# Performance work log

Hardware: AMD Instinct MI355X
Metric: run time of the kernel (lower is better)

## Reference

```python
import jax, jax.numpy as jnp
import numpy as np

B, H, S, D = 2, 16, 2048, 64


def setup_inputs() -> dict:
    key = jax.random.key(0)
    kq, kk, kv = jax.random.split(key, 3)
    Q = jax.random.normal(kq, (B, H, S, D), dtype=jnp.float32)
    K = jax.random.normal(kk, (B, H, S, D), dtype=jnp.float32)
    V = jax.random.normal(kv, (B, H, S, D), dtype=jnp.float32)
    scale = jnp.float32(1.0 / np.sqrt(D))
    # causal mask (1 = keep, 0 = masked), broadcast over batch/heads
    mask = jnp.tril(jnp.ones((S, S), dtype=jnp.int32))[None, None]
    return {"Q": Q, "K": K, "V": V, "scale": scale, "mask": mask}


def reference(Q, K, V, scale, mask):
    # scores: [B,H,S,S] -- intentionally materialized, matching the module
    scores = jnp.einsum("bhqd,bhkd->bhqk", Q, K) * scale
    scores = jnp.where(mask == 0, jnp.float32(-jnp.inf), scores)
    attention_weights = jax.nn.softmax(scores, axis=-1)
    # dropout is identity in eval mode (reference baseline is deterministic)
    output = jnp.einsum("bhqk,bhkd->bhqd", attention_weights, V)
    return output, attention_weights
```

## Files before the change

### kernel.cpp

```cpp
#include <hip/hip_runtime.h>
#include <hip/hip_bf16.h>

#define S_LEN 2048
#define D_DIM 64
#define BH    32
#define BQ    64
#define BK    64
#define NQT   (S_LEN/BQ)
#define KSTR  72
#define NEL   ((size_t)BH * S_LEN * D_DIM)

typedef __attribute__((ext_vector_type(4))) short  short4v;
typedef __attribute__((ext_vector_type(8))) short  short8;
typedef __attribute__((ext_vector_type(4))) float  floatx4;
typedef __attribute__((ext_vector_type(4))) unsigned int uintx4;

__device__ __forceinline__ unsigned short f2bf(float f) {
    unsigned int u = __builtin_bit_cast(unsigned int, f);
    u += 0x7FFFu + ((u >> 16) & 1u);
    return (unsigned short)(u >> 16);
}
__device__ __forceinline__ float bf2f(short s) {
    return __builtin_bit_cast(float, ((unsigned int)(unsigned short)s) << 16);
}

__device__ __forceinline__ short8 load8(const float* p) {
    floatx4 a = *(const floatx4*)p;
    floatx4 b = *(const floatx4*)(p + 4);
    short8 r;
    r[0]=(short)f2bf(a[0]); r[1]=(short)f2bf(a[1]); r[2]=(short)f2bf(a[2]); r[3]=(short)f2bf(a[3]);
    r[4]=(short)f2bf(b[0]); r[5]=(short)f2bf(b[1]); r[6]=(short)f2bf(b[2]); r[7]=(short)f2bf(b[3]);
    return r;
}
__device__ __forceinline__ short8 load8(const __hip_bfloat16* p) {
    return *(const short8*)p;
}
__device__ __forceinline__ void loadrow8(const float* p, unsigned short o[8]) {
    floatx4 a = *(const floatx4*)p, b = *(const floatx4*)(p + 4);
    o[0]=f2bf(a[0]); o[1]=f2bf(a[1]); o[2]=f2bf(a[2]); o[3]=f2bf(a[3]);
    o[4]=f2bf(b[0]); o[5]=f2bf(b[1]); o[6]=f2bf(b[2]); o[7]=f2bf(b[3]);
}
__device__ __forceinline__ void loadrow8(const __hip_bfloat16* p, unsigned short o[8]) {
    short8 v = *(const short8*)p;
#pragma unroll
    for (int j = 0; j < 8; ++j) o[j] = (unsigned short)v[j];
}

template<typename TIN>
__device__ __forceinline__ void prep_body(const TIN* __restrict__ Q, const TIN* __restrict__ K,
                                          const TIN* __restrict__ V,
                                          unsigned short* __restrict__ Qb,
                                          unsigned short* __restrict__ Kb,
                                          unsigned short* __restrict__ Vtg,
                                          unsigned short (*Lt)[KSTR])
{
    const int tid = threadIdx.x;
    const int bid = blockIdx.x;
    {
        size_t idx = ((size_t)bid * 256 + tid) * 16;
        *(short8*)(Qb + idx)     = load8(Q + idx);
        *(short8*)(Qb + idx + 8) = load8(Q + idx + 8);
        *(short8*)(Kb + idx)     = load8(K + idx);
        *(short8*)(Kb + idx + 8) = load8(K + idx + 8);
    }
    const int bh = bid >> 5, st = bid & 31;
    const TIN* Vb = V + ((size_t)bh * S_LEN + (size_t)st * 64) * D_DIM;
#pragma unroll
    for (int i = 0; i < 2; ++i) {
        int flat = tid * 8 + i * 2048;
        int r = flat >> 6, c = flat & 63;
        short8 v = load8(Vb + (size_t)r * D_DIM + c);
        *(short8*)(&Lt[r][c]) = v;
    }
    __syncthreads();
    unsigned short* Vh = Vtg + (size_t)bh * D_DIM * S_LEN;
#pragma unroll
    for (int i = 0; i < 4; ++i) {
        int flat = tid * 4 + i * 1024;
        int d = flat >> 6, sj = flat & 63;
        short4v o;
        o[0] = (short)Lt[sj+0][d]; o[1] = (short)Lt[sj+1][d];
        o[2] = (short)Lt[sj+2][d]; o[3] = (short)Lt[sj+3][d];
        *(short4v*)(Vh + (size_t)d * S_LEN + (size_t)st * 64 + sj) = o;
    }
}

__global__ __launch_bounds__(256)
void prep_kernel(const void* __restrict__ Q, const void* __restrict__ K,
                 const void* __restrict__ V, const void* __restrict__ scp,
                 unsigned short* __restrict__ Qb, unsigned short* __restrict__ Kb,
                 unsigned short* __restrict__ Vtg)
{
    __shared__ unsigned short Lt[64][KSTR];
    const unsigned int sw = *(const unsigned int*)scp;
    if ((sw & 0xFFFFu) == 0u)
        prep_body<float>((const float*)Q, (const float*)K, (const float*)V, Qb, Kb, Vtg, Lt);
    else
        prep_body<__hip_bfloat16>((const __hip_bfloat16*)Q, (const __hip_bfloat16*)K,
                                  (const __hip_bfloat16*)V, Qb, Kb, Vtg, Lt);
}

__device__ __forceinline__ void ldK(const unsigned short* Kh, int kk0, int tid, uintx4 r[2]) {
#pragma unroll
    for (int i = 0; i < 2; ++i)
        r[i] = *(const uintx4*)(Kh + (size_t)kk0 * D_DIM + tid * 8 + i * 2048);
}
__device__ __forceinline__ void ldV(const unsigned short* Vh, int kk0, int tid, uintx4 r[2]) {
#pragma unroll
    for (int i = 0; i < 2; ++i) {
        int flat = tid * 8 + i * 2048;
        r[i] = *(const uintx4*)(Vh + (size_t)(flat >> 6) * S_LEN + kk0 + (flat & 63));
    }
}
__device__ __forceinline__ void st2(unsigned short* dst, int tid, const uintx4 r[2]) {
#pragma unroll
    for (int i = 0; i < 2; ++i) {
        int flat = tid * 8 + i * 2048;
        *(uintx4*)(dst + (flat >> 6) * KSTR + (flat & 63)) = r[i];
    }
}

__global__ __launch_bounds__(256, 4)
void attn_fast(const unsigned short* __restrict__ Qb, const unsigned short* __restrict__ Kb,
               const unsigned short* __restrict__ Vtg, const void* __restrict__ scp,
               float* __restrict__ Out, float* __restrict__ W)
{
    __shared__ unsigned short Kl[2][BK * KSTR];
    __shared__ unsigned short Vl[2][D_DIM * KSTR];

    const int tid  = threadIdx.x;
    const int wave = tid >> 6;
    const int lane = tid & 63;
    const int quad = lane >> 4;
    const int lm   = lane & 15;
    const int idx  = blockIdx.x;
    const int bh   = idx & (BH - 1);
    const int qt   = (NQT - 1) - (idx >> 5);
    const int q0   = qt * BQ;

    const unsigned int sw = *(const unsigned int*)scp;
    const bool isf32 = ((sw & 0xFFFFu) == 0u);
    const float sc = isf32 ? __builtin_bit_cast(float, sw)
                           : __builtin_bit_cast(float, (sw & 0xFFFFu) << 16);
    const float sc2 = sc * 1.44269504088896f;

    float* Ob = Out + (size_t)bh * S_LEN * D_DIM;
    float* Wb = W   + (size_t)bh * S_LEN * S_LEN;
    const unsigned short* Qh = Qb  + (size_t)bh * S_LEN * D_DIM;
    const unsigned short* Kh = Kb  + (size_t)bh * S_LEN * D_DIM;
    const unsigned short* Vh = Vtg + (size_t)bh * D_DIM * S_LEN;

    {
        const int zc = S_LEN - (q0 + BQ);
        floatx4 z4 = {0.f, 0.f, 0.f, 0.f};
        for (int r = 0; r < BQ; ++r) {
            float* wr = Wb + (size_t)(q0 + r) * S_LEN + (q0 + BQ);
            for (int c = tid * 4; c < zc; c += 256 * 4)
                __builtin_nontemporal_store(z4, (floatx4*)(wr + c));
        }
    }

    const int qrow = q0 + wave * 16 + lm;
    const short8 qf0 = *(const short8*)(Qh + (size_t)qrow * D_DIM + quad * 8);
    const short8 qf1 = *(const short8*)(Qh + (size_t)qrow * D_DIM + 32 + quad * 8);

    {
        uintx4 kr[2];
        ldK(Kh, 0, tid, kr); st2(Kl[0], tid, kr);
    }
    __syncthreads();

    float ls0 = 0.f, ls1 = 0.f, ls2 = 0.f, ls3 = 0.f;
    for (int kt = 0; kt <= qt; ++kt) {
        const bool pre = (kt < qt);
        uintx4 kreg[2];
        if (pre) ldK(Kh, (kt + 1) * BK, tid, kreg);
        const unsigned short* Kc = Kl[kt & 1];
        const int kk0 = kt * BK;
        const bool diag = (kt == qt);
#pragma unroll
        for (int kkt = 0; kkt < 4; ++kkt) {
            floatx4 acc = {0.f, 0.f, 0.f, 0.f};
            short8 b0 = *(const short8*)(Kc + (kkt * 16 + lm) * KSTR + quad * 8);
            short8 b1 = *(const short8*)(Kc + (kkt * 16 + lm) * KSTR + 32 + quad * 8);
            acc = __builtin_amdgcn_mfma_f32_16x16x32_bf16(b0, qf0, acc, 0, 0, 0);
            acc = __builtin_amdgcn_mfma_f32_16x16x32_bf16(b1, qf1, acc, 0, 0, 0);
            float s0 = acc[0] * sc2, s1 = acc[1] * sc2;
            float s2 = acc[2] * sc2, s3 = acc[3] * sc2;
            if (diag) {
                int kg = kk0 + kkt * 16 + quad * 4;
                if (kg + 0 > qrow) s0 = -1e30f;
                if (kg + 1 > qrow) s1 = -1e30f;
                if (kg + 2 > qrow) s2 = -1e30f;
                if (kg + 3 > qrow) s3 = -1e30f;
            }
            ls0 += exp2f(s0); ls1 += exp2f(s1);
            ls2 += exp2f(s2); ls3 += exp2f(s3);
        }
        if (pre) st2(Kl[(kt + 1) & 1], tid, kreg);
        __syncthreads();
    }
    float lsum = (ls0 + ls1) + (ls2 + ls3);
    lsum += __shfl_xor(lsum, 16, 64);
    lsum += __shfl_xor(lsum, 32, 64);
    const float linv = 1.0f / lsum;

    {
        uintx4 kr[2], vr[2];
        ldK(Kh, 0, tid, kr); ldV(Vh, 0, tid, vr);
        st2(Kl[0], tid, kr); st2(Vl[0], tid, vr);
    }
    __syncthreads();

    floatx4 oacc[4];
#pragma unroll
    for (int dt = 0; dt < 4; ++dt) oacc[dt] = (floatx4){0.f, 0.f, 0.f, 0.f};

    for (int kt = 0; kt <= qt; ++kt) {
        const bool pre = (kt < qt);
        uintx4 kreg[2], vreg[2];
        if (pre) { ldK(Kh, (kt + 1) * BK, tid, kreg); ldV(Vh, (kt + 1) * BK, tid, vreg); }
        const unsigned short* Kc = Kl[kt & 1];
        const unsigned short* Vc = Vl[kt & 1];
        const int kk0 = kt * BK;
        const bool diag = (kt == qt);

        unsigned int dd[4][2];
#pragma unroll
        for (int kkt = 0; kkt < 4; ++kkt) {
            floatx4 acc = {0.f, 0.f, 0.f, 0.f};
            short8 b0 = *(const short8*)(Kc + (kkt * 16 + lm) * KSTR + quad * 8);
            short8 b1 = *(const short8*)(Kc + (kkt * 16 + lm) * KSTR + 32 + quad * 8);
            acc = __builtin_amdgcn_mfma_f32_16x16x32_bf16(b0, qf0, acc, 0, 0, 0);
            acc = __builtin_amdgcn_mfma_f32_16x16x32_bf16(b1, qf1, acc, 0, 0, 0);
            const int kg = kk0 + kkt * 16 + quad * 4;
            float s0 = acc[0] * sc2, s1 = acc[1] * sc2;
            float s2 = acc[2] * sc2, s3 = acc[3] * sc2;
            if (diag) {
                if (kg + 0 > qrow) s0 = -1e30f;
                if (kg + 1 > qrow) s1 = -1e30f;
                if (kg + 2 > qrow) s2 = -1e30f;
                if (kg + 3 > qrow) s3 = -1e30f;
            }
            float p0 = exp2f(s0) * linv, p1 = exp2f(s1) * linv;
            float p2 = exp2f(s2) * linv, p3 = exp2f(s3) * linv;
            floatx4 w4; w4[0] = p0; w4[1] = p1; w4[2] = p2; w4[3] = p3;
            __builtin_nontemporal_store(w4, (floatx4*)(Wb + (size_t)qrow * S_LEN + kg));
            asm("v_cvt_pk_bf16_f32 %0, %1, %2" : "=v"(dd[kkt][0]) : "v"(p0), "v"(p1));
            asm("v_cvt_pk_bf16_f32 %0, %1, %2" : "=v"(dd[kkt][1]) : "v"(p2), "v"(p3));
        }
#pragma unroll
        for (int c = 0; c < 2; ++c) {
            asm("v_permlane32_swap_b32 %0, %1" : "+v"(dd[2*c][0]), "+v"(dd[2*c+1][0]));
            asm("v_permlane32_swap_b32 %0, %1" : "+v"(dd[2*c][1]), "+v"(dd[2*c+1][1]));
            asm("v_permlane16_swap_b32 %0, %1" : "+v"(dd[2*c][0]), "+v"(dd[2*c+1][0]));
            asm("v_permlane16_swap_b32 %0, %1" : "+v"(dd[2*c][1]), "+v"(dd[2*c+1][1]));
        }
#pragma unroll
        for (int c = 0; c < 2; ++c) {
            uintx4 pv_;
            pv_[0] = dd[2*c][0]; pv_[1] = dd[2*c][1];
            pv_[2] = dd[2*c+1][0]; pv_[3] = dd[2*c+1][1];
            short8 pf = __builtin_bit_cast(short8, pv_);
#pragma unroll
            for (int dt = 0; dt < 4; ++dt) {
                short8 vf = *(const short8*)(Vc + (dt * 16 + lm) * KSTR + c * 32 + quad * 8);
                oacc[dt] = __builtin_amdgcn_mfma_f32_16x16x32_bf16(pf, vf, oacc[dt], 0, 0, 0);
            }
        }

        if (pre) {
            st2(Kl[(kt + 1) & 1], tid, kreg);
            st2(Vl[(kt + 1) & 1], tid, vreg);
            __syncthreads();
        }
    }

#pragma unroll
    for (int dt = 0; dt < 4; ++dt)
#pragma unroll
        for (int r = 0; r < 4; ++r)
            Ob[(size_t)(q0 + wave * 16 + quad * 4 + r) * D_DIM + dt * 16 + lm] = oacc[dt][r];
}

template<typename TIN>
__device__ __forceinline__ void stageK(const TIN* Kb, int kk0, __hip_bfloat16* Kl, int tid) {
    if constexpr (sizeof(TIN) == 4) {
#pragma unroll
        for (int i = 0; i < 4; ++i) {
            int flat = tid * 4 + i * 1024;
            int row = flat >> 6, col = flat & 63;
            floatx4 v = *(const floatx4*)((const float*)Kb + (size_t)(kk0 + row) * D_DIM + col);
            short4v s;
            s[0]=(short)f2bf(v[0]); s[1]=(short)f2bf(v[1]);
            s[2]=(short)f2bf(v[2]); s[3]=(short)f2bf(v[3]);
            *(short4v*)(&Kl[row * KSTR + col]) = s;
        }
    } else {
#pragma unroll
        for (int i = 0; i < 2; ++i) {
            int flat = tid * 8 + i * 2048;
            int row = flat >> 6, col = flat & 63;
            *(uintx4*)(&Kl[row * KSTR + col]) =
                *(const uintx4*)((const __hip_bfloat16*)Kb + (size_t)(kk0 + row) * D_DIM + col);
        }
    }
}

template<typename TIN>
__device__ __forceinline__ void attn_body(
    const TIN* __restrict__ Qb, const TIN* __restrict__ Kb, const TIN* __restrict__ Vb,
    float sc2, float* __restrict__ Ob, float* __restrict__ Wb,
    int q0, int qt, __hip_bfloat16* Kl, __hip_bfloat16* Vt, __hip_bfloat16* Plw)
{
    const int tid  = threadIdx.x;
    const int wave = tid >> 6;
    const int lane = tid & 63;
    const int quad = lane >> 4;
    const int lm   = lane & 15;

    const int qrow = q0 + wave * 16 + lm;
    short8 qfrag0 = load8(Qb + (size_t)qrow * D_DIM + quad * 8);
    short8 qfrag1 = load8(Qb + (size_t)qrow * D_DIM + 32 + quad * 8);

    float mrow[4], lrow[4];
#pragma unroll
    for (int r = 0; r < 4; ++r) { mrow[r] = -1e30f; lrow[r] = 0.f; }

    for (int kt = 0; kt <= qt; ++kt) {
        const int kk0 = kt * BK;
        __syncthreads();
        stageK(Kb, kk0, Kl, tid);
        __syncthreads();

        const bool diag = (kt == qt);
        float s[4][4];
#pragma unroll
        for (int kkt = 0; kkt < 4; ++kkt) {
            floatx4 acc = {0.f, 0.f, 0.f, 0.f};
            short8 b0 = *(const short8*)(&Kl[(kkt * 16 + lm) * KSTR + quad * 8]);
            short8 b1 = *(const short8*)(&Kl[(kkt * 16 + lm) * KSTR + 32 + quad * 8]);
            acc = __builtin_amdgcn_mfma_f32_16x16x32_bf16(qfrag0, b0, acc, 0, 0, 0);
            acc = __builtin_amdgcn_mfma_f32_16x16x32_bf16(qfrag1, b1, acc, 0, 0, 0);
#pragma unroll
            for (int r = 0; r < 4; ++r) s[kkt][r] = acc[r] * sc2;
            if (diag) {
                int colg = kk0 + kkt * 16 + lm;
#pragma unroll
                for (int r = 0; r < 4; ++r) {
                    int rowg = q0 + wave * 16 + quad * 4 + r;
                    if (colg > rowg) s[kkt][r] = -1e30f;
                }
            }
        }
#pragma unroll
        for (int r = 0; r < 4; ++r) {
            float mx = fmaxf(fmaxf(s[0][r], s[1][r]), fmaxf(s[2][r], s[3][r]));
#pragma unroll
            for (int off = 1; off < 16; off <<= 1)
                mx = fmaxf(mx, __shfl_xor(mx, off, 64));
            float mnew = fmaxf(mrow[r], mx);
            float p = exp2f(s[0][r] - mnew) + exp2f(s[1][r] - mnew) +
                      exp2f(s[2][r] - mnew) + exp2f(s[3][r] - mnew);
#pragma unroll
            for (int off = 1; off < 16; off <<= 1)
                p += __shfl_xor(p, off, 64);
            lrow[r] = lrow[r] * exp2f(mrow[r] - mnew) + p;
            mrow[r] = mnew;
        }
    }

    float inv_l[4];
#pragma unroll
    for (int r = 0; r < 4; ++r) inv_l[r] = 1.0f / lrow[r];

    floatx4 oacc[4];
#pragma unroll
    for (int dt = 0; dt < 4; ++dt) oacc[dt] = (floatx4){0.f, 0.f, 0.f, 0.f};

    for (int kt = 0; kt <= qt; ++kt) {
        const int kk0 = kt * BK;
        __syncthreads();
        stageK(Kb, kk0, Kl, tid);
        {
            int r = tid & 31, c = (tid >> 5) << 3;
            const TIN* v0 = Vb + (size_t)(kk0 + 2 * r) * D_DIM + c;
            unsigned short a[8], b[8];
            loadrow8(v0, a);
            loadrow8(v0 + D_DIM, b);
#pragma unroll
            for (int j = 0; j < 8; ++j) {
                unsigned int d = (unsigned int)a[j] | ((unsigned int)b[j] << 16);
                *(unsigned int*)(&Vt[(c + j) * KSTR + 2 * r]) = d;
            }
        }
        __syncthreads();

        const bool diag = (kt == qt);
        float s[4][4];
#pragma unroll
        for (int kkt = 0; kkt < 4; ++kkt) {
            floatx4 acc = {0.f, 0.f, 0.f, 0.f};
            short8 b0 = *(const short8*)(&Kl[(kkt * 16 + lm) * KSTR + quad * 8]);
            short8 b1 = *(const short8*)(&Kl[(kkt * 16 + lm) * KSTR + 32 + quad * 8]);
            acc = __builtin_amdgcn_mfma_f32_16x16x32_bf16(qfrag0, b0, acc, 0, 0, 0);
            acc = __builtin_amdgcn_mfma_f32_16x16x32_bf16(qfrag1, b1, acc, 0, 0, 0);
#pragma unroll
            for (int r = 0; r < 4; ++r) s[kkt][r] = acc[r] * sc2;
            if (diag) {
                int colg = kk0 + kkt * 16 + lm;
#pragma unroll
                for (int r = 0; r < 4; ++r) {
                    int rowg = q0 + wave * 16 + quad * 4 + r;
                    if (colg > rowg) s[kkt][r] = -1e30f;
                }
            }
        }
#pragma unroll
        for (int kkt = 0; kkt < 4; ++kkt) {
#pragma unroll
            for (int r = 0; r < 4; ++r) {
                float p = exp2f(s[kkt][r] - mrow[r]) * inv_l[r];
                Plw[(quad * 4 + r) * KSTR + kkt * 16 + lm] =
                    __builtin_bit_cast(__hip_bfloat16, f2bf(p));
            }
        }
        __asm__ volatile("s_waitcnt lgkmcnt(0)" ::: "memory");

        {
            int rr = lane >> 3, cc = (lane & 7) << 3;
            short8 w0 = *(const short8*)(&Plw[rr * KSTR + cc]);
            short8 w1 = *(const short8*)(&Plw[(8 + rr) * KSTR + cc]);
            float* wp0 = Wb + (size_t)(q0 + wave * 16 + rr) * S_LEN + kk0 + cc;
            float* wp1 = Wb + (size_t)(q0 + wave * 16 + 8 + rr) * S_LEN + kk0 + cc;
            floatx4 fa, fb;
#pragma unroll
            for (int j = 0; j < 4; ++j) { fa[j] = bf2f(w0[j]); fb[j] = bf2f(w0[4 + j]); }
            *(floatx4*)wp0 = fa; *(floatx4*)(wp0 + 4) = fb;
#pragma unroll
            for (int j = 0; j < 4; ++j) { fa[j] = bf2f(w1[j]); fb[j] = bf2f(w1[4 + j]); }
            *(floatx4*)wp1 = fa; *(floatx4*)(wp1 + 4) = fb;
        }
#pragma unroll
        for (int c = 0; c < 2; ++c) {
            short8 pf = *(const short8*)(&Plw[lm * KSTR + c * 32 + quad * 8]);
#pragma unroll
            for (int dt = 0; dt < 4; ++dt) {
                short8 vf = *(const short8*)(&Vt[(dt * 16 + lm) * KSTR + c * 32 + quad * 8]);
                oacc[dt] = __builtin_amdgcn_mfma_f32_16x16x32_bf16(pf, vf, oacc[dt], 0, 0, 0);
            }
        }
    }

#pragma unroll
    for (int dt = 0; dt < 4; ++dt)
#pragma unroll
        for (int r = 0; r < 4; ++r)
            Ob[(size_t)(q0 + wave * 16 + quad * 4 + r) * D_DIM + dt * 16 + lm] = oacc[dt][r];
}

__global__ __launch_bounds__(256, 4)
void attn_kernel(const void* __restrict__ Q, const void* __restrict__ K,
                 const void* __restrict__ V, const void* __restrict__ scp,
                 float* __restrict__ Out, float* __restrict__ W)
{
    __shared__ __hip_bfloat16 Kl[BK * KSTR];
    __shared__ __hip_bfloat16 Vt[D_DIM * KSTR];
    __shared__ __hip_bfloat16 Pl[4][16 * KSTR];

    const int tid  = threadIdx.x;
    const int wave = tid >> 6;
    const int idx  = blockIdx.x;
    const int bh   = idx & (BH - 1);
    const int qt   = (NQT - 1) - (idx >> 5);
    const int q0   = qt * BQ;

    const size_t bqd = (size_t)bh * S_LEN * D_DIM;
    float* Ob = Out + bqd;
    float* Wb = W + (size_t)bh * S_LEN * S_LEN;

    const unsigned int sw = *(const unsigned int*)scp;
    const bool isf32 = ((sw & 0xFFFFu) == 0u);
    const float sc = isf32 ? __builtin_bit_cast(float, sw)
                           : __builtin_bit_cast(float, (sw & 0xFFFFu) << 16);
    const float sc2 = sc * 1.44269504088896f;

    {
        const int zc = S_LEN - (q0 + BQ);
        floatx4 z4 = {0.f, 0.f, 0.f, 0.f};
        for (int r = 0; r < BQ; ++r) {
            float* wr = Wb + (size_t)(q0 + r) * S_LEN + (q0 + BQ);
            for (int c = tid * 4; c < zc; c += 256 * 4)
                *(floatx4*)(wr + c) = z4;
        }
    }

    if (isf32)
        attn_body<float>((const float*)Q + bqd, (const float*)K + bqd,
                         (const float*)V + bqd, sc2, Ob, Wb, q0, qt, Kl, Vt, Pl[wave]);
    else
        attn_body<__hip_bfloat16>((const __hip_bfloat16*)Q + bqd, (const __hip_bfloat16*)K + bqd,
                                  (const __hip_bfloat16*)V + bqd, sc2, Ob, Wb, q0, qt, Kl, Vt, Pl[wave]);
}

extern "C" void kernel_launch(void* const* d_in, const int* in_sizes, int n_in,
                              void* d_out, int out_size, void* d_ws, size_t ws_size,
                              hipStream_t stream) {
    float* Outp = (float*)d_out;
    float* Wp   = Outp + NEL;

    const size_t need = NEL * 3 * sizeof(unsigned short);
    if (d_ws != nullptr && ws_size >= need) {
        unsigned short* Qb  = (unsigned short*)d_ws;
        unsigned short* Kb  = Qb + NEL;
        unsigned short* Vtg = Kb + NEL;
        prep_kernel<<<dim3(NQT * BH), dim3(256), 0, stream>>>(
            d_in[0], d_in[1], d_in[2], d_in[3], Qb, Kb, Vtg);
        attn_fast<<<dim3(NQT * BH), dim3(256), 0, stream>>>(
            Qb, Kb, Vtg, d_in[3], Outp, Wp);
    } else {
        attn_kernel<<<dim3(NQT * BH), dim3(256), 0, stream>>>(
            d_in[0], d_in[1], d_in[2], d_in[3], Outp, Wp);
    }
}
```

Baseline: 679.2 us.

## Pair light and heavy causal query tiles per block to share K/V loads

Each block now handles two query tiles, j and NQT-1-j, for the same head, and walks the K/V tiles once for both. This halves the grid and balances causal work across blocks. Each staged K/V tile is reused for both query tiles, cutting global-to-LDS traffic. It raises register pressure (launch bounds drop from 4 to 2 blocks per CU) and leaves fewer, longer blocks, which may reduce latency hiding.

Result: faster. 659.4 us (-2.9%).

```diff
diff --git a/kernel.cpp b/kernel.cpp
--- a/kernel.cpp
+++ b/kernel.cpp
@@ -7,6 +7,7 @@
 #define BQ    64
 #define BK    64
 #define NQT   (S_LEN/BQ)
+#define NPAIR (NQT/2)
 #define KSTR  72
 #define NEL   ((size_t)BH * S_LEN * D_DIM)
 
@@ -120,10 +121,10 @@
     }
 }
 
-__global__ __launch_bounds__(256, 4)
-void attn_fast(const unsigned short* __restrict__ Qb, const unsigned short* __restrict__ Kb,
-               const unsigned short* __restrict__ Vtg, const void* __restrict__ scp,
-               float* __restrict__ Out, float* __restrict__ W)
+__global__ __launch_bounds__(256, 2)
+void attn_joint(const unsigned short* __restrict__ Qb, const unsigned short* __restrict__ Kb,
+                const unsigned short* __restrict__ Vtg, const void* __restrict__ scp,
+                float* __restrict__ Out, float* __restrict__ W)
 {
     __shared__ unsigned short Kl[2][BK * KSTR];
     __shared__ unsigned short Vl[2][D_DIM * KSTR];
@@ -135,8 +136,10 @@
     const int lm   = lane & 15;
     const int idx  = blockIdx.x;
     const int bh   = idx & (BH - 1);
-    const int qt   = (NQT - 1) - (idx >> 5);
-    const int q0   = qt * BQ;
+    const int j    = idx >> 5;
+    const int qtA  = j;
+    const int qtB  = (NQT - 1) - j;
+    const int q0A  = qtA * BQ, q0B = qtB * BQ;
 
     const unsigned int sw = *(const unsigned int*)scp;
     const bool isf32 = ((sw & 0xFFFFu) == 0u);
@@ -151,18 +154,27 @@
     const unsigned short* Vh = Vtg + (size_t)bh * D_DIM * S_LEN;
 
     {
-        const int zc = S_LEN - (q0 + BQ);
         floatx4 z4 = {0.f, 0.f, 0.f, 0.f};
+        const int zcA = S_LEN - (q0A + BQ);
         for (int r = 0; r < BQ; ++r) {
-            float* wr = Wb + (size_t)(q0 + r) * S_LEN + (q0 + BQ);
-            for (int c = tid * 4; c < zc; c += 256 * 4)
+            float* wr = Wb + (size_t)(q0A + r) * S_LEN + (q0A + BQ);
+            for (int c = tid * 4; c < zcA; c += 256 * 4)
                 __builtin_nontemporal_store(z4, (floatx4*)(wr + c));
         }
-    }
-
-    const int qrow = q0 + wave * 16 + lm;
-    const short8 qf0 = *(const short8*)(Qh + (size_t)qrow * D_DIM + quad * 8);
-    const short8 qf1 = *(const short8*)(Qh + (size_t)qrow * D_DIM + 32 + quad * 8);
+        const int zcB = S_LEN - (q0B + BQ);
+        for (int r = 0; r < BQ; ++r) {
+            float* wr = Wb + (size_t)(q0B + r) * S_LEN + (q0B + BQ);
+            for (int c = tid * 4; c < zcB; c += 256 * 4)
+                __builtin_nontemporal_store(z4, (floatx4*)(wr + c));
+        }
+    }
+
+    const int qrowA = q0A + wave * 16 + lm;
+    const int qrowB = q0B + wave * 16 + lm;
+    const short8 qfA0 = *(const short8*)(Qh + (size_t)qrowA * D_DIM + quad * 8);
+    const short8 qfA1 = *(const short8*)(Qh + (size_t)qrowA * D_DIM + 32 + quad * 8);
+    const short8 qfB0 = *(const short8*)(Qh + (size_t)qrowB * D_DIM + quad * 8);
+    const short8 qfB1 = *(const short8*)(Qh + (size_t)qrowB * D_DIM + 32 + quad * 8);
 
     {
         uintx4 kr[2];
@@ -170,40 +182,61 @@
     }
     __syncthreads();
 
-    float ls0 = 0.f, ls1 = 0.f, ls2 = 0.f, ls3 = 0.f;
-    for (int kt = 0; kt <= qt; ++kt) {
-        const bool pre = (kt < qt);
+    float lsA0 = 0.f, lsA1 = 0.f, lsA2 = 0.f, lsA3 = 0.f;
+    float lsB0 = 0.f, lsB1 = 0.f, lsB2 = 0.f, lsB3 = 0.f;
+    for (int kt = 0; kt <= qtB; ++kt) {
+        const bool pre  = (kt < qtB);
+        const bool actA = (kt <= qtA);
         uintx4 kreg[2];
         if (pre) ldK(Kh, (kt + 1) * BK, tid, kreg);
         const unsigned short* Kc = Kl[kt & 1];
         const int kk0 = kt * BK;
-        const bool diag = (kt == qt);
+        const bool diagA = (kt == qtA), diagB = (kt == qtB);
 #pragma unroll
         for (int kkt = 0; kkt < 4; ++kkt) {
-            floatx4 acc = {0.f, 0.f, 0.f, 0.f};
             short8 b0 = *(const short8*)(Kc + (kkt * 16 + lm) * KSTR + quad * 8);
             short8 b1 = *(const short8*)(Kc + (kkt * 16 + lm) * KSTR + 32 + quad * 8);
-            acc = __builtin_amdgcn_mfma_f32_16x16x32_bf16(b0, qf0, acc, 0, 0, 0);
-            acc = __builtin_amdgcn_mfma_f32_16x16x32_bf16(b1, qf1, acc, 0, 0, 0);
-            float s0 = acc[0] * sc2, s1 = acc[1] * sc2;
-            float s2 = acc[2] * sc2, s3 = acc[3] * sc2;
-            if (diag) {
-                int kg = kk0 + kkt * 16 + quad * 4;
-                if (kg + 0 > qrow) s0 = -1e30f;
-                if (kg + 1 > qrow) s1 = -1e30f;
-                if (kg + 2 > qrow) s2 = -1e30f;
-                if (kg + 3 > qrow) s3 = -1e30f;
-            }
-            ls0 += exp2f(s0); ls1 += exp2f(s1);
-            ls2 += exp2f(s2); ls3 += exp2f(s3);
+            const int kg = kk0 + kkt * 16 + quad * 4;
+            {
+                floatx4 acc = {0.f, 0.f, 0.f, 0.f};
+                acc = __builtin_amdgcn_mfma_f32_16x16x32_bf16(b0, qfB0, acc, 0, 0, 0);
+                acc = __builtin_amdgcn_mfma_f32_16x16x32_bf16(b1, qfB1, acc, 0, 0, 0);
+                float s0 = acc[0] * sc2, s1 = acc[1] * sc2;
+                float s2 = acc[2] * sc2, s3 = acc[3] * sc2;
+                if (diagB) {
+                    if (kg + 0 > qrowB) s0 = -1e30f;
+                    if (kg + 1 > qrowB) s1 = -1e30f;
+                    if (kg + 2 > qrowB) s2 = -1e30f;
+                    if (kg + 3 > qrowB) s3 = -1e30f;
+                }
+                lsB0 += exp2f(s0); lsB1 += exp2f(s1);
+                lsB2 += exp2f(s2); lsB3 += exp2f(s3);
+            }
+            if (actA) {
+                floatx4 acc = {0.f, 0.f, 0.f, 0.f};
+                acc = __builtin_amdgcn_mfma_f32_16x16x32_bf16(b0, qfA0, acc, 0, 0, 0);
+                acc = __builtin_amdgcn_mfma_f32_16x16x32_bf16(b1, qfA1, acc, 0, 0, 0);
+                float s0 = acc[0] * sc2, s1 = acc[1] * sc2;
+                float s2 = acc[2] * sc2, s3 = acc[3] * sc2;
+                if (diagA) {
+                    if (kg + 0 > qrowA) s0 = -1e30f;
+                    if (kg + 1 > qrowA) s1 = -1e30f;
+                    if (kg + 2 > qrowA) s2 = -1e30f;
+                    if (kg + 3 > qrowA) s3 = -1e30f;
+                }
+                lsA0 += exp2f(s0); lsA1 += exp2f(s1);
+                lsA2 += exp2f(s2); lsA3 += exp2f(s3);
+            }
         }
         if (pre) st2(Kl[(kt + 1) & 1], tid, kreg);
         __syncthreads();
     }
-    float lsum = (ls0 + ls1) + (ls2 + ls3);
-    lsum += __shfl_xor(lsum, 16, 64);
-    lsum += __shfl_xor(lsum, 32, 64);
-    const float linv = 1.0f / lsum;
+    float lsA = (lsA0 + lsA1) + (lsA2 + lsA3);
+    float lsB = (lsB0 + lsB1) + (lsB2 + lsB3);
+    lsA += __shfl_xor(lsA, 16, 64);  lsA += __shfl_xor(lsA, 32, 64);
+    lsB += __shfl_xor(lsB, 16, 64);  lsB += __shfl_xor(lsB, 32, 64);
+    const float linvA = 1.0f / lsA;
+    const float linvB = 1.0f / lsB;
 
     {
         uintx4 kr[2], vr[2];
@@ -212,60 +245,100 @@
     }
     __syncthreads();
 
-    floatx4 oacc[4];
-#pragma unroll
-    for (int dt = 0; dt < 4; ++dt) oacc[dt] = (floatx4){0.f, 0.f, 0.f, 0.f};
-
-    for (int kt = 0; kt <= qt; ++kt) {
-        const bool pre = (kt < qt);
+    floatx4 oaccA[4], oaccB[4];
+#pragma unroll
+    for (int dt = 0; dt < 4; ++dt) {
+        oaccA[dt] = (floatx4){0.f, 0.f, 0.f, 0.f};
+        oaccB[dt] = (floatx4){0.f, 0.f, 0.f, 0.f};
+    }
+
+    for (int kt = 0; kt <= qtB; ++kt) {
+        const bool pre  = (kt < qtB);
+        const bool actA = (kt <= qtA);
         uintx4 kreg[2], vreg[2];
         if (pre) { ldK(Kh, (kt + 1) * BK, tid, kreg); ldV(Vh, (kt + 1) * BK, tid, vreg); }
         const unsigned short* Kc = Kl[kt & 1];
         const unsigned short* Vc = Vl[kt & 1];
         const int kk0 = kt * BK;
-        const bool diag = (kt == qt);
-
-        unsigned int dd[4][2];
+        const bool diagA = (kt == qtA), diagB = (kt == qtB);
+
+        unsigned int ddA[4][2], ddB[4][2];
 #pragma unroll
         for (int kkt = 0; kkt < 4; ++kkt) {
-            floatx4 acc = {0.f, 0.f, 0.f, 0.f};
             short8 b0 = *(const short8*)(Kc + (kkt * 16 + lm) * KSTR + quad * 8);
             short8 b1 = *(const short8*)(Kc + (kkt * 16 + lm) * KSTR + 32 + quad * 8);
-            acc = __builtin_amdgcn_mfma_f32_16x16x32_bf16(b0, qf0, acc, 0, 0, 0);
-            acc = __builtin_amdgcn_mfma_f32_16x16x32_bf16(b1, qf1, acc, 0, 0, 0);
             const int kg = kk0 + kkt * 16 + quad * 4;
-            float s0 = acc[0] * sc2, s1 = acc[1] * sc2;
-            float s2 = acc[2] * sc2, s3 = acc[3] * sc2;
-            if (diag) {
-                if (kg + 0 > qrow) s0 = -1e30f;
-                if (kg + 1 > qrow) s1 = -1e30f;
-                if (kg + 2 > qrow) s2 = -1e30f;
-                if (kg + 3 > qrow) s3 = -1e30f;
-            }
-            float p0 = exp2f(s0) * linv, p1 = exp2f(s1) * linv;
-            float p2 = exp2f(s2) * linv, p3 = exp2f(s3) * linv;
-            floatx4 w4; w4[0] = p0; w4[1] = p1; w4[2] = p2; w4[3] = p3;
-            __builtin_nontemporal_store(w4, (floatx4*)(Wb + (size_t)qrow * S_LEN + kg));
-            asm("v_cvt_pk_bf16_f32 %0, %1, %2" : "=v"(dd[kkt][0]) : "v"(p0), "v"(p1));
-            asm("v_cvt_pk_bf16_f32 %0, %1, %2" : "=v"(dd[kkt][1]) : "v"(p2), "v"(p3));
+            {
+                floatx4 acc = {0.f, 0.f, 0.f, 0.f};
+                acc = __builtin_amdgcn_mfma_f32_16x16x32_bf16(b0, qfB0, acc, 0, 0, 0);
+                acc = __builtin_amdgcn_mfma_f32_16x16x32_bf16(b1, qfB1, acc, 0, 0, 0);
+                float s0 = acc[0] * sc2, s1 = acc[1] * sc2;
+                float s2 = acc[2] * sc2, s3 = acc[3] * sc2;
+                if (diagB) {
+                    if (kg + 0 > qrowB) s0 = -1e30f;
+                    if (kg + 1 > qrowB) s1 = -1e30f;
+                    if (kg + 2 > qrowB) s2 = -1e30f;
+                    if (kg + 3 > qrowB) s3 = -1e30f;
+                }
+                float p0 = exp2f(s0) * linvB, p1 = exp2f(s1) * linvB;
+                float p2 = exp2f(s2) * linvB, p3 = exp2f(s3) * linvB;
+                floatx4 w4; w4[0] = p0; w4[1] = p1; w4[2] = p2; w4[3] = p3;
+                __builtin_nontemporal_store(w4, (floatx4*)(Wb + (size_t)qrowB * S_LEN + kg));
+                asm("v_cvt_pk_bf16_f32 %0, %1, %2" : "=v"(ddB[kkt][0]) : "v"(p0), "v"(p1));
+                asm("v_cvt_pk_bf16_f32 %0, %1, %2" : "=v"(ddB[kkt][1]) : "v"(p2), "v"(p3));
+            }
+            if (actA) {
+                floatx4 acc = {0.f, 0.f, 0.f, 0.f};
+                acc = __builtin_amdgcn_mfma_f32_16x16x32_bf16(b0, qfA0, acc, 0, 0, 0);
+                acc = __builtin_amdgcn_mfma_f32_16x16x32_bf16(b1, qfA1, acc, 0, 0, 0);
+                float s0 = acc[0] * sc2, s1 = acc[1] * sc2;
+                float s2 = acc[2] * sc2, s3 = acc[3] * sc2;
+                if (diagA) {
+                    if (kg + 0 > qrowA) s0 = -1e30f;
+                    if (kg + 1 > qrowA) s1 = -1e30f;
+                    if (kg + 2 > qrowA) s2 = -1e30f;
+                    if (kg + 3 > qrowA) s3 = -1e30f;
+                }
+                float p0 = exp2f(s0) * linvA, p1 = exp2f(s1) * linvA;
+                float p2 = exp2f(s2) * linvA, p3 = exp2f(s3) * linvA;
+                floatx4 w4; w4[0] = p0; w4[1] = p1; w4[2] = p2; w4[3] = p3;
+                __builtin_nontemporal_store(w4, (floatx4*)(Wb + (size_t)qrowA * S_LEN + kg));
+                asm("v_cvt_pk_bf16_f32 %0, %1, %2" : "=v"(ddA[kkt][0]) : "v"(p0), "v"(p1));
+                asm("v_cvt_pk_bf16_f32 %0, %1, %2" : "=v"(ddA[kkt][1]) : "v"(p2), "v"(p3));
+            }
         }
 #pragma unroll
         for (int c = 0; c < 2; ++c) {
-            asm("v_permlane32_swap_b32 %0, %1" : "+v"(dd[2*c][0]), "+v"(dd[2*c+1][0]));
-            asm("v_permlane32_swap_b32 %0, %1" : "+v"(dd[2*c][1]), "+v"(dd[2*c+1][1]));
-            asm("v_permlane16_swap_b32 %0, %1" : "+v"(dd[2*c][0]), "+v"(dd[2*c+1][0]));
-            asm("v_permlane16_swap_b32 %0, %1" : "+v"(dd[2*c][1]), "+v"(dd[2*c+1][1]));
+            asm("v_permlane32_swap_b32 %0, %1" : "+v"(ddB[2*c][0]), "+v"(ddB[2*c+1][0]));
+            asm("v_permlane32_swap_b32 %0, %1" : "+v"(ddB[2*c][1]), "+v"(ddB[2*c+1][1]));
+            asm("v_permlane16_swap_b32 %0, %1" : "+v"(ddB[2*c][0]), "+v"(ddB[2*c+1][0]));
+            asm("v_permlane16_swap_b32 %0, %1" : "+v"(ddB[2*c][1]), "+v"(ddB[2*c+1][1]));
+        }
+        if (actA) {
+#pragma unroll
+            for (int c = 0; c < 2; ++c) {
+                asm("v_permlane32_swap_b32 %0, %1" : "+v"(ddA[2*c][0]), "+v"(ddA[2*c+1][0]));
+                asm("v_permlane32_swap_b32 %0, %1" : "+v"(ddA[2*c][1]), "+v"(ddA[2*c+1][1]));
+                asm("v_permlane16_swap_b32 %0, %1" : "+v"(ddA[2*c][0]), "+v"(ddA[2*c+1][0]));
+                asm("v_permlane16_swap_b32 %0, %1" : "+v"(ddA[2*c][1]), "+v"(ddA[2*c+1][1]));
+            }
         }
 #pragma unroll
         for (int c = 0; c < 2; ++c) {
-            uintx4 pv_;
-            pv_[0] = dd[2*c][0]; pv_[1] = dd[2*c][1];
-            pv_[2] = dd[2*c+1][0]; pv_[3] = dd[2*c+1][1];
-            short8 pf = __builtin_bit_cast(short8, pv_);
+            uintx4 pb_;
+            pb_[0] = ddB[2*c][0]; pb_[1] = ddB[2*c][1];
+            pb_[2] = ddB[2*c+1][0]; pb_[3] = ddB[2*c+1][1];
+            short8 pfB = __builtin_bit_cast(short8, pb_);
+            uintx4 pa_;
+            pa_[0] = ddA[2*c][0]; pa_[1] = ddA[2*c][1];
+            pa_[2] = ddA[2*c+1][0]; pa_[3] = ddA[2*c+1][1];
+            short8 pfA = __builtin_bit_cast(short8, pa_);
 #pragma unroll
             for (int dt = 0; dt < 4; ++dt) {
                 short8 vf = *(const short8*)(Vc + (dt * 16 + lm) * KSTR + c * 32 + quad * 8);
-                oacc[dt] = __builtin_amdgcn_mfma_f32_16x16x32_bf16(pf, vf, oacc[dt], 0, 0, 0);
+                oaccB[dt] = __builtin_amdgcn_mfma_f32_16x16x32_bf16(pfB, vf, oaccB[dt], 0, 0, 0);
+                if (actA)
+                    oaccA[dt] = __builtin_amdgcn_mfma_f32_16x16x32_bf16(pfA, vf, oaccA[dt], 0, 0, 0);
             }
         }
 
@@ -279,8 +352,10 @@
 #pragma unroll
     for (int dt = 0; dt < 4; ++dt)
 #pragma unroll
-        for (int r = 0; r < 4; ++r)
-            Ob[(size_t)(q0 + wave * 16 + quad * 4 + r) * D_DIM + dt * 16 + lm] = oacc[dt][r];
+        for (int r = 0; r < 4; ++r) {
+            Ob[(size_t)(q0B + wave * 16 + quad * 4 + r) * D_DIM + dt * 16 + lm] = oaccB[dt][r];
+            Ob[(size_t)(q0A + wave * 16 + quad * 4 + r) * D_DIM + dt * 16 + lm] = oaccA[dt][r];
+        }
 }
 
 template<typename TIN>
@@ -516,7 +591,7 @@
         unsigned short* Vtg = Kb + NEL;
         prep_kernel<<<dim3(NQT * BH), dim3(256), 0, stream>>>(
             d_in[0], d_in[1], d_in[2], d_in[3], Qb, Kb, Vtg);
-        attn_fast<<<dim3(NQT * BH), dim3(256), 0, stream>>>(
+        attn_joint<<<dim3(NPAIR * BH), dim3(256), 0, stream>>>(
             Qb, Kb, Vtg, d_in[3], Outp, Wp);
     } else {
         attn_kernel<<<dim3(NQT * BH), dim3(256), 0, stream>>>(
```
